# Kernel optimization log

Measured on AMD Instinct MI355X. Metric: run time of the kernel, lower is better.

The kernel has to match this reference:

```python
import jax, jax.numpy as jnp
import numpy as np

IN_FEATURES = [32, 32]
OUT_FEATURES = [64, 64]
RANKS = [16, 16, 16, 16]


def _make_cores(key):
    dims = IN_FEATURES + OUT_FEATURES
    ranks = RANKS
    # init scale as in the torch module
    var = 2 ** (1.0 / len(dims)) / np.prod(np.power(np.array(ranks) + np.array(IN_FEATURES + IN_FEATURES), 1.0 / len(dims)))
    ub = float(np.sqrt(3.0 * var))
    ranks_ext = [ranks[-1]] + list(ranks)
    cores = []
    for i in range(len(dims)):
        key, k = jax.random.split(key)
        cores.append(jax.random.uniform(k, (ranks_ext[i], dims[i], ranks_ext[i + 1]), jnp.float32, -ub, ub))
    return cores, key


def setup_inputs() -> dict:
    key = jax.random.key(0)
    cores, key = _make_cores(key)
    key, kx, kb = jax.random.split(key, 3)
    x = jax.random.normal(kx, (8192, int(np.prod(IN_FEATURES))), jnp.float32)
    bias = jax.random.normal(kb, (int(np.prod(OUT_FEATURES)),), jnp.float32)
    return {"x": x, "core0": cores[0], "core1": cores[1], "core2": cores[2], "core3": cores[3], "bias": bias}


def reference(x, core0, core1, core2, core3, bias):
    # Tensor-ring contraction to build the dense weight, then linear.
    # core shapes: (16,32,16), (16,32,16), (16,64,16), (16,64,16)
    w = jnp.tensordot(core0, core1, axes=([2], [0]))        # (r, i0, i1, r)
    w = jnp.tensordot(w, core2, axes=([3], [0]))            # (r, i0, i1, o0, r)
    # last core: contract w's trailing rank with core axis 0 AND w's leading
    # rank with core's trailing rank (closes the ring) -> (i0, i1, o0, o1)
    w = jnp.tensordot(w, core3, axes=([4, 0], [0, 2]))
    d_out = int(np.prod(OUT_FEATURES))
    w = w.reshape(d_out, -1)                                # (4096, 1024)
    return x @ w.T + bias
```

## Files before the change

### kernel.cpp

```cpp
#include <hip/hip_runtime.h>
#include <hip/hip_bf16.h>
#include <stdint.h>

typedef unsigned short ushort_t;
typedef __attribute__((ext_vector_type(8))) short short8;
typedef __attribute__((ext_vector_type(4))) float floatx4;

__device__ __forceinline__ ushort_t f2bf(float f) {
    union { float f; unsigned u; } v; v.f = f;
    unsigned r = v.u + 0x7fffu + ((v.u >> 16) & 1u);
    return (ushort_t)(r >> 16);
}

__device__ __forceinline__ void async16(ushort_t* lds, const ushort_t* g) {
    __builtin_amdgcn_global_load_lds(
        (const __attribute__((address_space(1))) unsigned int*)g,
        (__attribute__((address_space(3))) unsigned int*)lds, 16, 0, 0);
}


__global__ __launch_bounds__(256) void prep_all(const float* __restrict__ x,
                                                const float* __restrict__ c0,
                                                const float* __restrict__ c1,
                                                const float* __restrict__ c2,
                                                const float* __restrict__ c3,
                                                ushort_t* __restrict__ Xb,
                                                ushort_t* __restrict__ V,
                                                ushort_t* __restrict__ A2b) {
    const int blk = blockIdx.x, t = threadIdx.x;
    if (blk < 8192) {
        int i = blk * 256 + t;
        float4 v = ((const float4*)x)[i];
        ushort4 r;
        r.x = f2bf(v.x); r.y = f2bf(v.y); r.z = f2bf(v.z); r.w = f2bf(v.w);
        ((ushort4*)Xb)[i] = r;
    } else if (blk < 12288) {
        int id = (blk - 8192) * 256 + t;
        int c = id & 1023, kp = id >> 10;
        int b = kp >> 8, k = kp & 255;
        int r0 = k >> 4, r2 = k & 15;
        int o0 = b * 16 + (c >> 6), o1 = c & 63;
        const float* p2 = c2 + (r2 * 64 + o0) * 16;
        const float* p3 = c3 + o1 * 16 + r0;
        float s = 0.f;
#pragma unroll
        for (int r3 = 0; r3 < 16; r3++) s += p2[r3] * p3[r3 * 1024];
        V[id] = f2bf(s);
    } else {
        int id = (blk - 12288) * 256 + t;
        int k = id & 255, a = id >> 8;
        int r0 = k >> 4, r2 = k & 15;
        int i0 = a >> 5, i1 = a & 31;
        const float* p0 = c0 + (r0 * 32 + i0) * 16;
        const float* p1 = c1 + i1 * 16 + r2;
        float s = 0.f;
#pragma unroll
        for (int r1 = 0; r1 < 16; r1++) s += p0[r1] * p1[r1 * 512];
        A2b[id] = f2bf(s);
    }
}

__global__ __launch_bounds__(256) void gemm_z(const ushort_t* __restrict__ Xb,
                                              const ushort_t* __restrict__ V,
                                              ushort_t* __restrict__ Z) {
    __shared__ ushort_t As[128 * 32];
    __shared__ ushort_t Bs[64 * 32];
    const int t = threadIdx.x;
    const int row0 = blockIdx.x * 128;
    const int col0 = blockIdx.y * 64;
    const int w = t >> 6, l = t & 63;
    const int wm = w >> 1, wn = w & 1;
    const int quad = l >> 4, ln = l & 15;

    floatx4 acc[4][2] = {};

    const ushort_t* aSrc = Xb + (size_t)(row0 + (t >> 2)) * 1024 + (t & 3) * 8;
    const ushort_t* bSrc = V  + (size_t)(col0 + (t >> 2)) * 1024 + (t & 3) * 8;

    for (int kk = 0; kk < 1024; kk += 32) {
        async16(&As[t * 8],        aSrc + kk);
        async16(&As[2048 + t * 8], aSrc + 64 * 1024 + kk);
        async16(&Bs[t * 8],        bSrc + kk);
        __syncthreads();

        short8 a[4], b[2];
#pragma unroll
        for (int ti = 0; ti < 4; ti++)
            a[ti] = *(const short8*)&As[(wm * 64 + ti * 16 + ln) * 32 + quad * 8];
#pragma unroll
        for (int tj = 0; tj < 2; tj++)
            b[tj] = *(const short8*)&Bs[(wn * 32 + tj * 16 + ln) * 32 + quad * 8];
#pragma unroll
        for (int ti = 0; ti < 4; ti++)
#pragma unroll
            for (int tj = 0; tj < 2; tj++)
                acc[ti][tj] = __builtin_amdgcn_mfma_f32_16x16x32_bf16(
                    a[ti], b[tj], acc[ti][tj], 0, 0, 0);
        __syncthreads();
    }

#pragma unroll
    for (int tj = 0; tj < 2; tj++) {
        const int n = col0 + wn * 32 + tj * 16 + ln;
#pragma unroll
        for (int ti = 0; ti < 4; ti++) {
            const int m = row0 + wm * 64 + ti * 16 + quad * 4;
#pragma unroll
            for (int r = 0; r < 4; r++)
                Z[(size_t)(m + r) * 1024 + n] = f2bf(acc[ti][tj][r]);
        }
    }
}

__global__ __launch_bounds__(256) void gemm_out(const ushort_t* __restrict__ Z,
                                                const ushort_t* __restrict__ A2b,
                                                const float* __restrict__ bias,
                                                float* __restrict__ out) {
    __shared__ ushort_t As[128 * 32];
    __shared__ ushort_t Bs[128 * 32];
    const int t = threadIdx.x;
    const int row0 = blockIdx.x * 128;
    const int a0 = (blockIdx.y >> 2) * 128;
    const int b  = blockIdx.y & 3;
    const int w = t >> 6, l = t & 63;
    const int wm = w >> 1, wn = w & 1;
    const int quad = l >> 4, ln = l & 15;

    floatx4 acc[4][4] = {};

    const ushort_t* aSrc = Z   + (size_t)(row0 + (t >> 2)) * 1024 + b * 256 + (t & 3) * 8;
    const ushort_t* bSrc = A2b + (size_t)(a0   + (t >> 2)) * 256  + (t & 3) * 8;

    for (int kk = 0; kk < 256; kk += 32) {
        async16(&As[t * 8],        aSrc + kk);
        async16(&As[2048 + t * 8], aSrc + 64 * 1024 + kk);
        async16(&Bs[t * 8],        bSrc + kk);
        async16(&Bs[2048 + t * 8], bSrc + 64 * 256 + kk);
        __syncthreads();

        short8 a[4], bb[4];
#pragma unroll
        for (int ti = 0; ti < 4; ti++)
            a[ti] = *(const short8*)&As[(wm * 64 + ti * 16 + ln) * 32 + quad * 8];
#pragma unroll
        for (int tj = 0; tj < 4; tj++)
            bb[tj] = *(const short8*)&Bs[(wn * 64 + tj * 16 + ln) * 32 + quad * 8];
#pragma unroll
        for (int ti = 0; ti < 4; ti++)
#pragma unroll
            for (int tj = 0; tj < 4; tj++)
                acc[ti][tj] = __builtin_amdgcn_mfma_f32_16x16x32_bf16(
                    a[ti], bb[tj], acc[ti][tj], 0, 0, 0);
        __syncthreads();
    }

#pragma unroll
    for (int tj = 0; tj < 4; tj++) {
        const int aIdx = a0 + wn * 64 + tj * 16 + ln;
        const int j = aIdx * 4 + b;
        const float bv = bias[j];
#pragma unroll
        for (int ti = 0; ti < 4; ti++) {
            const int m = row0 + wm * 64 + ti * 16 + quad * 4;
            float* o = out + (size_t)m * 4096 + j;
#pragma unroll
            for (int r = 0; r < 4; r++)
                o[(size_t)r * 4096] = acc[ti][tj][r] + bv;
        }
    }
}

extern "C" void kernel_launch(void* const* d_in, const int* in_sizes, int n_in,
                              void* d_out, int out_size, void* d_ws, size_t ws_size,
                              hipStream_t stream) {
    const float* x    = (const float*)d_in[0];
    const float* c0   = (const float*)d_in[1];
    const float* c1   = (const float*)d_in[2];
    const float* c2   = (const float*)d_in[3];
    const float* c3   = (const float*)d_in[4];
    const float* bias = (const float*)d_in[5];
    float* out = (float*)d_out;

    char* ws = (char*)d_ws;
    ushort_t* Xb  = (ushort_t*)ws;
    ushort_t* V   = (ushort_t*)(ws + (16u << 20));
    ushort_t* A2b = (ushort_t*)(ws + (18u << 20));
    ushort_t* Zb  = (ushort_t*)(ws + (20u << 20));

    hipLaunchKernelGGL(prep_all, dim3(13312), dim3(256), 0, stream,
                       x, c0, c1, c2, c3, Xb, V, A2b);
    hipLaunchKernelGGL(gemm_z,   dim3(64, 16), dim3(256), 0, stream, Xb, V, Zb);
    hipLaunchKernelGGL(gemm_out, dim3(64, 32), dim3(256), 0, stream, Zb, A2b, bias, out);
}
```

Measured before the change: 287.3 us.

## Widen gemm_z tile and restructure gemm_out for coalesced float4 stores

gemm_z moves from a 128x64 to a 128x128 output tile, doubling B-tile reuse and halving the grid. gemm_out now has each block handle all four b-slices for 64 'a' columns. It keeps the A2 slice resident in padded LDS and loads four Z sub-tiles per k step. This lets each thread write float4 outputs across the interleaved b dimension instead of 4-byte strided stores, and load bias as a float4. The cost is more accumulator registers and LDS per block, which lowers occupancy, and fewer blocks in both GEMMs.

Result: faster. 255.3 us (-11.2%).

```diff
diff --git a/kernel.cpp b/kernel.cpp
--- a/kernel.cpp
+++ b/kernel.cpp
@@ -64,15 +64,15 @@
                                               const ushort_t* __restrict__ V,
                                               ushort_t* __restrict__ Z) {
     __shared__ ushort_t As[128 * 32];
-    __shared__ ushort_t Bs[64 * 32];
+    __shared__ ushort_t Bs[128 * 32];
     const int t = threadIdx.x;
     const int row0 = blockIdx.x * 128;
-    const int col0 = blockIdx.y * 64;
+    const int col0 = blockIdx.y * 128;
     const int w = t >> 6, l = t & 63;
     const int wm = w >> 1, wn = w & 1;
     const int quad = l >> 4, ln = l & 15;
 
-    floatx4 acc[4][2] = {};
+    floatx4 acc[4][4] = {};
 
     const ushort_t* aSrc = Xb + (size_t)(row0 + (t >> 2)) * 1024 + (t & 3) * 8;
     const ushort_t* bSrc = V  + (size_t)(col0 + (t >> 2)) * 1024 + (t & 3) * 8;
@@ -81,27 +81,28 @@
         async16(&As[t * 8],        aSrc + kk);
         async16(&As[2048 + t * 8], aSrc + 64 * 1024 + kk);
         async16(&Bs[t * 8],        bSrc + kk);
-        __syncthreads();
-
-        short8 a[4], b[2];
+        async16(&Bs[2048 + t * 8], bSrc + 64 * 1024 + kk);
+        __syncthreads();
+
+        short8 a[4], b[4];
 #pragma unroll
         for (int ti = 0; ti < 4; ti++)
             a[ti] = *(const short8*)&As[(wm * 64 + ti * 16 + ln) * 32 + quad * 8];
 #pragma unroll
-        for (int tj = 0; tj < 2; tj++)
-            b[tj] = *(const short8*)&Bs[(wn * 32 + tj * 16 + ln) * 32 + quad * 8];
+        for (int tj = 0; tj < 4; tj++)
+            b[tj] = *(const short8*)&Bs[(wn * 64 + tj * 16 + ln) * 32 + quad * 8];
 #pragma unroll
         for (int ti = 0; ti < 4; ti++)
 #pragma unroll
-            for (int tj = 0; tj < 2; tj++)
+            for (int tj = 0; tj < 4; tj++)
                 acc[ti][tj] = __builtin_amdgcn_mfma_f32_16x16x32_bf16(
                     a[ti], b[tj], acc[ti][tj], 0, 0, 0);
         __syncthreads();
     }
 
 #pragma unroll
-    for (int tj = 0; tj < 2; tj++) {
-        const int n = col0 + wn * 32 + tj * 16 + ln;
+    for (int tj = 0; tj < 4; tj++) {
+        const int n = col0 + wn * 64 + tj * 16 + ln;
 #pragma unroll
         for (int ti = 0; ti < 4; ti++) {
             const int m = row0 + wm * 64 + ti * 16 + quad * 4;
@@ -116,56 +117,69 @@
                                                 const ushort_t* __restrict__ A2b,
                                                 const float* __restrict__ bias,
                                                 float* __restrict__ out) {
-    __shared__ ushort_t As[128 * 32];
-    __shared__ ushort_t Bs[128 * 32];
+    __shared__ ushort_t Zs[4 * 128 * 32];
+    __shared__ ushort_t A2s[64 * 264];
     const int t = threadIdx.x;
     const int row0 = blockIdx.x * 128;
-    const int a0 = (blockIdx.y >> 2) * 128;
-    const int b  = blockIdx.y & 3;
+    const int a0 = blockIdx.y * 64;
     const int w = t >> 6, l = t & 63;
     const int wm = w >> 1, wn = w & 1;
     const int quad = l >> 4, ln = l & 15;
 
-    floatx4 acc[4][4] = {};
-
-    const ushort_t* aSrc = Z   + (size_t)(row0 + (t >> 2)) * 1024 + b * 256 + (t & 3) * 8;
-    const ushort_t* bSrc = A2b + (size_t)(a0   + (t >> 2)) * 256  + (t & 3) * 8;
+    floatx4 acc[4][2][4] = {};
+
+#pragma unroll
+    for (int q = 0; q < 8; q++) {
+        int g = q * 2048 + t * 8;
+        int r = g >> 8, cidx = g & 255;
+        short8 v = *(const short8*)(A2b + (size_t)(a0 + r) * 256 + cidx);
+        *(short8*)&A2s[r * 264 + cidx] = v;
+    }
+
+    const ushort_t* zSrc = Z + (size_t)(row0 + (t >> 2)) * 1024 + (t & 3) * 8;
 
     for (int kk = 0; kk < 256; kk += 32) {
-        async16(&As[t * 8],        aSrc + kk);
-        async16(&As[2048 + t * 8], aSrc + 64 * 1024 + kk);
-        async16(&Bs[t * 8],        bSrc + kk);
-        async16(&Bs[2048 + t * 8], bSrc + 64 * 256 + kk);
-        __syncthreads();
-
-        short8 a[4], bb[4];
-#pragma unroll
-        for (int ti = 0; ti < 4; ti++)
-            a[ti] = *(const short8*)&As[(wm * 64 + ti * 16 + ln) * 32 + quad * 8];
-#pragma unroll
-        for (int tj = 0; tj < 4; tj++)
-            bb[tj] = *(const short8*)&Bs[(wn * 64 + tj * 16 + ln) * 32 + quad * 8];
-#pragma unroll
-        for (int ti = 0; ti < 4; ti++)
-#pragma unroll
-            for (int tj = 0; tj < 4; tj++)
-                acc[ti][tj] = __builtin_amdgcn_mfma_f32_16x16x32_bf16(
-                    a[ti], bb[tj], acc[ti][tj], 0, 0, 0);
-        __syncthreads();
-    }
-
-#pragma unroll
-    for (int tj = 0; tj < 4; tj++) {
-        const int aIdx = a0 + wn * 64 + tj * 16 + ln;
-        const int j = aIdx * 4 + b;
-        const float bv = bias[j];
+#pragma unroll
+        for (int b = 0; b < 4; b++) {
+            async16(&Zs[b * 4096 + t * 8],        zSrc + b * 256 + kk);
+            async16(&Zs[b * 4096 + 2048 + t * 8], zSrc + 64 * 1024 + b * 256 + kk);
+        }
+        __syncthreads();
+
+        short8 bb[2];
+#pragma unroll
+        for (int tj = 0; tj < 2; tj++)
+            bb[tj] = *(const short8*)&A2s[(wn * 32 + tj * 16 + ln) * 264 + kk + quad * 8];
+#pragma unroll
+        for (int b = 0; b < 4; b++) {
+#pragma unroll
+            for (int ti = 0; ti < 4; ti++) {
+                short8 av = *(const short8*)&Zs[b * 4096 + (wm * 64 + ti * 16 + ln) * 32 + quad * 8];
+#pragma unroll
+                for (int tj = 0; tj < 2; tj++)
+                    acc[ti][tj][b] = __builtin_amdgcn_mfma_f32_16x16x32_bf16(
+                        av, bb[tj], acc[ti][tj][b], 0, 0, 0);
+            }
+        }
+        __syncthreads();
+    }
+
+#pragma unroll
+    for (int tj = 0; tj < 2; tj++) {
+        const int aIdx = a0 + wn * 32 + tj * 16 + ln;
+        const float4 bv = *(const float4*)(bias + aIdx * 4);
 #pragma unroll
         for (int ti = 0; ti < 4; ti++) {
-            const int m = row0 + wm * 64 + ti * 16 + quad * 4;
-            float* o = out + (size_t)m * 4096 + j;
-#pragma unroll
-            for (int r = 0; r < 4; r++)
-                o[(size_t)r * 4096] = acc[ti][tj][r] + bv;
+#pragma unroll
+            for (int r = 0; r < 4; r++) {
+                const int s = row0 + wm * 64 + ti * 16 + quad * 4 + r;
+                float4 o;
+                o.x = acc[ti][tj][0][r] + bv.x;
+                o.y = acc[ti][tj][1][r] + bv.y;
+                o.z = acc[ti][tj][2][r] + bv.z;
+                o.w = acc[ti][tj][3][r] + bv.w;
+                *(float4*)(out + (size_t)s * 4096 + aIdx * 4) = o;
+            }
         }
     }
 }
@@ -189,6 +203,6 @@
 
     hipLaunchKernelGGL(prep_all, dim3(13312), dim3(256), 0, stream,
                        x, c0, c1, c2, c3, Xb, V, A2b);
-    hipLaunchKernelGGL(gemm_z,   dim3(64, 16), dim3(256), 0, stream, Xb, V, Zb);
-    hipLaunchKernelGGL(gemm_out, dim3(64, 32), dim3(256), 0, stream, Zb, A2b, bias, out);
-}
+    hipLaunchKernelGGL(gemm_z,   dim3(64, 8),  dim3(256), 0, stream, Xb, V, Zb);
+    hipLaunchKernelGGL(gemm_out, dim3(64, 16), dim3(256), 0, stream, Zb, A2b, bias, out);
+}
```
